# Kernel tuning notes

Measured on AMD Instinct MI355X. Metric: run time of the kernel, lower is better.

Reference implementation:

```python
import jax, jax.numpy as jnp
import numpy as np

B, NF, FD, ND, C, K, L = 32, 64, 64, 256, 8, 6, 2  # batch, num_frames(feat), fused_dim, nodes, edge channels, neighbors, layers


def setup_inputs() -> dict:
    key = jax.random.key(0)
    ks = jax.random.split(key, 6)
    s = lambda k, shape: jax.random.normal(k, shape, jnp.float32) * 0.05
    return {
        "fused": jax.random.normal(ks[0], (B, NF, FD), jnp.float32),
        "w1": s(ks[1], (NF, FD, FD)),
        "b1": jnp.zeros((NF, 1, FD), jnp.float32),
        "w2": s(ks[2], (NF, FD, ND)),
        "b2": jnp.zeros((NF, 1, ND), jnp.float32),
        "edge_qk_w": s(ks[3], (2 * C * NF, NF)),
        "ga_qk_w": s(ks[4], (L, 2 * NF, NF)),
        "ga_qk_b": jnp.zeros((L, 2 * NF), jnp.float32),
        "ga_w": jnp.ones((L, 1, C), jnp.float32),
    }


def _spec_norm(w):
    # per-node spectral normalization (torch does this in-place under no_grad)
    n = jax.lax.stop_gradient(jnp.linalg.norm(w, ord=2, axis=(1, 2), keepdims=True))
    return w / jnp.clip(n, 1e-6, None)


def _forward(fused, w1, b1, w2, b2, edge_qk_w, ga_qk_w, ga_qk_b, ga_w):
    scale = NF ** -0.5
    # --- MultiNodeMlp (per-frame node-wise MLP) ---
    h = jnp.einsum('bni,nij->bnj', fused, _spec_norm(w1)) + b1[:, 0]
    h = jax.nn.gelu(h, approximate=False)
    conv = jnp.einsum('bni,nio->bno', h, _spec_norm(w2)) + b2[:, 0]  # [B,NF,ND]
    x = conv.transpose(0, 2, 1)  # node features [B,ND,NF]

    # --- EdgeLayer: multi-channel attention + top-k clip + double normalization ---
    qk = (x @ edge_qk_w.T).reshape(B, ND, 2, C, NF)
    q = qk[:, :, 0].transpose(0, 2, 1, 3)  # [B,C,ND,NF]
    k = qk[:, :, 1].transpose(0, 2, 1, 3)
    attn = jax.nn.softmax(jnp.einsum('bcnf,bcmf->bcnm', q, k) * scale, axis=-1)
    sum_edge = jax.lax.stop_gradient(attn).sum(axis=1)            # [B,ND,ND]
    top_idx = jax.lax.top_k(sum_edge, K)[1]                       # [B,ND,K]
    onehot = jnp.clip(jax.nn.one_hot(top_idx, ND, dtype=attn.dtype).sum(axis=2), 0.0, 1.0)
    mask = jnp.maximum(onehot, jnp.eye(ND, dtype=attn.dtype))[:, None]  # [B,1,ND,ND]
    masked = mask * attn
    nr = masked / (masked.sum(-1, keepdims=True) + 1e-6)
    nc = nr / (nr.sum(-2, keepdims=True) + 1e-6)
    edge = jnp.einsum('bcnd,bcmd->bcnm', nr, nc)                  # norm_row @ norm_col^T

    # --- LipschitzGraph: residual invertible graph attention layers ---
    eye = jnp.eye(NF, dtype=x.dtype)
    for l in range(L):
        W, bqk, wch = ga_qk_w[l], ga_qk_b[l], ga_w[l]
        xs = jax.nn.sigmoid(jax.nn.elu(x))
        qkx = xs @ W.T + bqk                                       # [B,ND,2NF]
        qg, kg = qkx[..., :NF], qkx[..., NF:]
        a = jax.nn.softmax(jnp.einsum('bnf,bmf->bnm', qg, kg) * scale, axis=-1)
        ne = a[:, None] * edge                                     # [B,C,ND,ND]
        ne = ne / (ne.sum(-1, keepdims=True) + 1e-6)
        ne = jnp.einsum('bcnd,c->bnd', ne, (wch / wch.sum())[0])
        dot = W[:NF] @ W[NF:].T * scale
        lip = jax.lax.stop_gradient(jnp.linalg.norm(eye + 2.0 * dot, ord=2)) + 5.0
        x = x + (ne @ xs) / lip
    return x


def reference(fused, w1, b1, w2, b2, edge_qk_w, ga_qk_w, ga_qk_b, ga_w):
    return _forward(fused, w1, b1, w2, b2, edge_qk_w, ga_qk_w, ga_qk_b, ga_w)
```

## Files before the change

kernel.cpp:

```cpp
#include <hip/hip_runtime.h>
#include <float.h>
#include <math.h>


typedef short bf8t __attribute__((ext_vector_type(8)));
typedef float f4t __attribute__((ext_vector_type(4)));

static __device__ __forceinline__ unsigned short f2bf(float x) {
  union { float f; unsigned u; } v; v.f = x;
  unsigned r = (v.u + 0x7FFFu + ((v.u >> 16) & 1u)) >> 16;
  return (unsigned short)r;
}
static __device__ __forceinline__ float bf2f(unsigned short s) {
  union { unsigned u; float f; } v; v.u = ((unsigned)s) << 16; return v.f;
}
static __device__ __forceinline__ float bf2f_lo(unsigned u) {
  union { unsigned u; float f; } v; v.u = u << 16; return v.f;
}
static __device__ __forceinline__ float bf2f_hi(unsigned u) {
  union { unsigned u; float f; } v; v.u = u & 0xFFFF0000u; return v.f;
}
static __device__ __forceinline__ float dot3_pair(unsigned uqh, unsigned uql,
                                                  unsigned ukh, unsigned ukl) {
  float s = bf2f_lo(uqh) * (bf2f_lo(ukh) + bf2f_lo(ukl)) + bf2f_lo(uql) * bf2f_lo(ukh);
  s += bf2f_hi(uqh) * (bf2f_hi(ukh) + bf2f_hi(ukl)) + bf2f_hi(uql) * bf2f_hi(ukh);
  return s;
}
static __device__ __forceinline__ void split8(const float* __restrict__ p,
                                              bf8t* hi, bf8t* lo) {
  float4 v0 = *(const float4*)(p);
  float4 v1 = *(const float4*)(p + 4);
  float v[8] = {v0.x, v0.y, v0.z, v0.w, v1.x, v1.y, v1.z, v1.w};
#pragma unroll
  for (int j = 0; j < 8; j++) {
    unsigned short h = f2bf(v[j]);
    (*hi)[j] = (short)h;
    (*lo)[j] = (short)f2bf(v[j] - bf2f(h));
  }
}

#define SPAD 68

static __device__ __forceinline__ void mm_mfma(
    const float* __restrict__ A, const float* __restrict__ B,
    float* __restrict__ C, int t, float scale, int addI, int transposeStore) {
  int wv = t >> 6, l = t & 63;
  int m16 = l & 15, quad = l >> 4;
  bf8t ah[2], al[2];
  const float* ap = A + (size_t)(16 * wv + m16) * SPAD + quad * 8;
  split8(ap, &ah[0], &al[0]);
  split8(ap + 32, &ah[1], &al[1]);
  f4t acc[4];
#pragma unroll
  for (int ct = 0; ct < 4; ct++) {
    bf8t bh[2], bl[2];
    const float* bp = B + (size_t)(ct * 16 + m16) * SPAD + quad * 8;
    split8(bp, &bh[0], &bl[0]);
    split8(bp + 32, &bh[1], &bl[1]);
    f4t a = (f4t){0.f, 0.f, 0.f, 0.f};
    a = __builtin_amdgcn_mfma_f32_16x16x32_bf16(al[0], bh[0], a, 0, 0, 0);
    a = __builtin_amdgcn_mfma_f32_16x16x32_bf16(ah[0], bl[0], a, 0, 0, 0);
    a = __builtin_amdgcn_mfma_f32_16x16x32_bf16(ah[0], bh[0], a, 0, 0, 0);
    a = __builtin_amdgcn_mfma_f32_16x16x32_bf16(al[1], bh[1], a, 0, 0, 0);
    a = __builtin_amdgcn_mfma_f32_16x16x32_bf16(ah[1], bl[1], a, 0, 0, 0);
    a = __builtin_amdgcn_mfma_f32_16x16x32_bf16(ah[1], bh[1], a, 0, 0, 0);
    acc[ct] = a;
  }
#pragma unroll
  for (int ct = 0; ct < 4; ct++)
#pragma unroll
    for (int j = 0; j < 4; j++) {
      int i0 = 16 * wv + quad * 4 + j;
      int j0 = ct * 16 + m16;
      float v = acc[ct][j] * scale + ((addI && i0 == j0) ? 1.0f : 0.0f);
      if (transposeStore) C[(size_t)j0 * SPAD + i0] = v;
      else C[(size_t)i0 * SPAD + j0] = v;
    }
}

static __device__ __forceinline__ void mm_sq_norm(
    const float* __restrict__ A, float* __restrict__ C, int t,
    float* __restrict__ redm) {
  int wv = t >> 6, l = t & 63;
  int m16 = l & 15, quad = l >> 4;
  bf8t ah[2], al[2];
  const float* ap = A + (size_t)(16 * wv + m16) * SPAD + quad * 8;
  split8(ap, &ah[0], &al[0]);
  split8(ap + 32, &ah[1], &al[1]);
  f4t acc[4];
#pragma unroll
  for (int ct = 0; ct < 4; ct++) {
    bf8t bh[2], bl[2];
    const float* bp = A + (size_t)(ct * 16 + m16) * SPAD + quad * 8;
    split8(bp, &bh[0], &bl[0]);
    split8(bp + 32, &bh[1], &bl[1]);
    f4t a = (f4t){0.f, 0.f, 0.f, 0.f};
    a = __builtin_amdgcn_mfma_f32_16x16x32_bf16(al[0], bh[0], a, 0, 0, 0);
    a = __builtin_amdgcn_mfma_f32_16x16x32_bf16(ah[0], bl[0], a, 0, 0, 0);
    a = __builtin_amdgcn_mfma_f32_16x16x32_bf16(ah[0], bh[0], a, 0, 0, 0);
    a = __builtin_amdgcn_mfma_f32_16x16x32_bf16(al[1], bh[1], a, 0, 0, 0);
    a = __builtin_amdgcn_mfma_f32_16x16x32_bf16(ah[1], bl[1], a, 0, 0, 0);
    a = __builtin_amdgcn_mfma_f32_16x16x32_bf16(ah[1], bh[1], a, 0, 0, 0);
    acc[ct] = a;
  }
  float mx = 0.f;
#pragma unroll
  for (int ct = 0; ct < 4; ct++)
#pragma unroll
    for (int j = 0; j < 4; j++) mx = fmaxf(mx, fabsf(acc[ct][j]));
#pragma unroll
  for (int m = 1; m < 64; m <<= 1) mx = fmaxf(mx, __shfl_xor(mx, m, 64));
  if (l == 0) redm[wv] = mx;
  __syncthreads();
  float gmx = fmaxf(fmaxf(redm[0], redm[1]), fmaxf(redm[2], redm[3]));
  float sc = 1.0f / fmaxf(gmx, 1e-30f);
#pragma unroll
  for (int ct = 0; ct < 4; ct++)
#pragma unroll
    for (int j = 0; j < 4; j++)
      C[(size_t)(16 * wv + quad * 4 + j) * SPAD + ct * 16 + m16] = acc[ct][j] * sc;
}

static __device__ __forceinline__ void gram_mfma(
    const float* __restrict__ Ag, int ncols, float* __restrict__ S,
    float* __restrict__ G, int t) {
  int wv = t >> 6, l = t & 63;
  int m16 = l & 15, quad = l >> 4;
  f4t acc[4];
#pragma unroll
  for (int ct = 0; ct < 4; ct++) acc[ct] = (f4t){0.f, 0.f, 0.f, 0.f};
  for (int cc = 0; cc < ncols; cc += 64) {
    if (cc) __syncthreads();
    for (int i = t; i < 1024; i += 256) {
      int r = i >> 4, qq = i & 15;
      float4 v = *(const float4*)(Ag + (size_t)r * ncols + cc + 4 * qq);
      *(float4*)(S + (size_t)r * SPAD + 4 * qq) = v;
    }
    __syncthreads();
    bf8t ah[2], al[2];
    const float* ap = S + (size_t)(16 * wv + m16) * SPAD + quad * 8;
    split8(ap, &ah[0], &al[0]);
    split8(ap + 32, &ah[1], &al[1]);
#pragma unroll
    for (int ct = 0; ct < 4; ct++) {
      bf8t bh[2], bl[2];
      const float* bp = S + (size_t)(ct * 16 + m16) * SPAD + quad * 8;
      split8(bp, &bh[0], &bl[0]);
      split8(bp + 32, &bh[1], &bl[1]);
      f4t a = acc[ct];
      a = __builtin_amdgcn_mfma_f32_16x16x32_bf16(al[0], bh[0], a, 0, 0, 0);
      a = __builtin_amdgcn_mfma_f32_16x16x32_bf16(ah[0], bl[0], a, 0, 0, 0);
      a = __builtin_amdgcn_mfma_f32_16x16x32_bf16(ah[0], bh[0], a, 0, 0, 0);
      a = __builtin_amdgcn_mfma_f32_16x16x32_bf16(al[1], bh[1], a, 0, 0, 0);
      a = __builtin_amdgcn_mfma_f32_16x16x32_bf16(ah[1], bl[1], a, 0, 0, 0);
      a = __builtin_amdgcn_mfma_f32_16x16x32_bf16(ah[1], bh[1], a, 0, 0, 0);
      acc[ct] = a;
    }
  }
  __syncthreads();
#pragma unroll
  for (int ct = 0; ct < 4; ct++)
#pragma unroll
    for (int j = 0; j < 4; j++)
      G[(size_t)(16 * wv + quad * 4 + j) * SPAD + ct * 16 + m16] = acc[ct][j];
}

static __device__ __forceinline__ float power_rayleigh(
    const float* __restrict__ G4m, const float* __restrict__ Gm, int iters, int i) {
  float row[64];
#pragma unroll
  for (int j = 0; j < 16; j++)
    *(float4*)(row + 4 * j) = *(const float4*)(G4m + (size_t)i * SPAD + 4 * j);
  float v = 1.0f + 0.3f * sinf(7.0f * (float)(i + 1));
  for (int it = 0; it < iters; it++) {
    float u0 = 0.f, u1 = 0.f, u2 = 0.f, u3 = 0.f;
#pragma unroll
    for (int j = 0; j < 16; j++) {
      u0 += row[4 * j + 0] * __shfl(v, 4 * j + 0, 64);
      u1 += row[4 * j + 1] * __shfl(v, 4 * j + 1, 64);
      u2 += row[4 * j + 2] * __shfl(v, 4 * j + 2, 64);
      u3 += row[4 * j + 3] * __shfl(v, 4 * j + 3, 64);
    }
    float u = (u0 + u1) + (u2 + u3);
    float ss = u * u;
#pragma unroll
    for (int m = 1; m < 64; m <<= 1) ss += __shfl_xor(ss, m, 64);
    v = u * rsqrtf(fmaxf(ss, 1e-30f));
  }
  float rowg[64];
#pragma unroll
  for (int j = 0; j < 16; j++)
    *(float4*)(rowg + 4 * j) = *(const float4*)(Gm + (size_t)i * SPAD + 4 * j);
  float u0 = 0.f, u1 = 0.f, u2 = 0.f, u3 = 0.f;
#pragma unroll
  for (int j = 0; j < 16; j++) {
    u0 += rowg[4 * j + 0] * __shfl(v, 4 * j + 0, 64);
    u1 += rowg[4 * j + 1] * __shfl(v, 4 * j + 1, 64);
    u2 += rowg[4 * j + 2] * __shfl(v, 4 * j + 2, 64);
    u3 += rowg[4 * j + 3] * __shfl(v, 4 * j + 3, 64);
  }
  float u = (u0 + u1) + (u2 + u3);
  float d = v * u;
#pragma unroll
  for (int m = 1; m < 64; m <<= 1) d += __shfl_xor(d, m, 64);
  return d;
}

__global__ __launch_bounds__(256) void speclip_kernel(
    const float* __restrict__ w1, const float* __restrict__ w2,
    const float* __restrict__ gaw, float* __restrict__ invsig1,
    float* __restrict__ invsig2, float* __restrict__ lipv) {
  __shared__ float Sa[64 * SPAD];
  __shared__ float Sb[64 * SPAD];
  __shared__ float G[64 * SPAD];
  __shared__ float redm[4];
  int t = threadIdx.x;
  int blk = blockIdx.x;
  if (blk < 128) {
    int n = blk & 63;
    const float* A = (blk < 64) ? (w1 + (size_t)n * 4096) : (w2 + (size_t)n * 16384);
    int ncols = (blk < 64) ? 64 : 256;
    gram_mfma(A, ncols, Sa, G, t);
    __syncthreads();
    mm_mfma(G, G, Sa, t, 1.f, 0, 0);
    __syncthreads();
    mm_sq_norm(Sa, Sb, t, redm);  __syncthreads();
    mm_sq_norm(Sb, Sa, t, redm);  __syncthreads();
    mm_sq_norm(Sa, Sb, t, redm);  __syncthreads();
    mm_sq_norm(Sb, Sa, t, redm);  __syncthreads();
    mm_sq_norm(Sa, Sb, t, redm);  __syncthreads();
    mm_sq_norm(Sb, Sa, t, redm);  __syncthreads();
    if (t < 64) {
      float d = power_rayleigh(Sa, G, 2, t);
      if (t == 0) {
        float sg = sqrtf(fmaxf(d, 0.f));
        float inv = 1.0f / fmaxf(sg, 1e-6f);
        if (blk < 64) invsig1[n] = inv; else invsig2[n] = inv;
      }
    }
  } else {
    int l = blk - 128;
    const float* Wb = gaw + (size_t)l * 8192;
    for (int i = t; i < 1024; i += 256) {
      int r = i >> 4, qq = i & 15;
      *(float4*)(Sa + (size_t)r * SPAD + 4 * qq) = *(const float4*)(Wb + r * 64 + 4 * qq);
      *(float4*)(Sb + (size_t)r * SPAD + 4 * qq) = *(const float4*)(Wb + 4096 + r * 64 + 4 * qq);
    }
    __syncthreads();
    mm_mfma(Sa, Sb, G, t, 0.25f, 1, 1);
    __syncthreads();
    mm_mfma(G, G, Sa, t, 1.f, 0, 0);
    __syncthreads();
    mm_sq_norm(Sa, Sb, t, redm);  __syncthreads();
    mm_sq_norm(Sb, G, t, redm);   __syncthreads();
    mm_sq_norm(G, Sb, t, redm);   __syncthreads();
    mm_sq_norm(Sb, G, t, redm);   __syncthreads();
    mm_sq_norm(G, Sb, t, redm);   __syncthreads();
    mm_sq_norm(Sb, G, t, redm);   __syncthreads();
    if (t < 64) {
      float d = power_rayleigh(G, Sa, 2, t);
      if (t == 0) lipv[l] = sqrtf(fmaxf(d, 0.f)) + 5.0f;
    }
  }
}

__global__ __launch_bounds__(256) void h_kernel(
    const float* __restrict__ fused, const float* __restrict__ w1,
    const float* __restrict__ b1, const float* __restrict__ invsig1,
    float* __restrict__ h) {
  __shared__ float fr[256];
  int t = threadIdx.x;
  int blk = blockIdx.x;
  int ng = blk & 15;
  fr[t] = fused[(size_t)blk * 256 + t];
  __syncthreads();
  int nl = t >> 6, j = t & 63;
  int n = ng * 4 + nl;
  float is1 = invsig1[n];
  const float* fp = fr + nl * 64;
  const float* wp = w1 + (size_t)n * 4096 + j;
  float acc = 0.f;
  for (int i = 0; i < 64; i++) acc += fp[i] * wp[i * 64];
  acc = acc * is1 + b1[n * 64 + j];
  float g = 0.5f * acc * (1.0f + erff(acc * 0.70710678118654752440f));
  h[(size_t)blk * 256 + t] = g;
}

__global__ __launch_bounds__(256) void conv_kernel(
    const float* __restrict__ h, const float* __restrict__ w2,
    const float* __restrict__ b2, const float* __restrict__ invsig2,
    float* __restrict__ x) {
  __shared__ float hr[4][64];
  int t = threadIdx.x;
  int blk = blockIdx.x;
  int b = blk >> 4, ng = blk & 15;
  int n0 = ng * 4;
  {
    int r = t >> 6, i = t & 63;
    hr[r][i] = h[((size_t)b * 64 + n0 + r) * 64 + i];
  }
  __syncthreads();
  const float* w0p = w2 + ((size_t)(n0 + 0) * 64) * 256 + t;
  const float* w1p = w2 + ((size_t)(n0 + 1) * 64) * 256 + t;
  const float* w2p = w2 + ((size_t)(n0 + 2) * 64) * 256 + t;
  const float* w3p = w2 + ((size_t)(n0 + 3) * 64) * 256 + t;
  float a0 = 0.f, a1 = 0.f, a2 = 0.f, a3 = 0.f;
  for (int i = 0; i < 64; i++) {
    a0 += hr[0][i] * w0p[(size_t)i * 256];
    a1 += hr[1][i] * w1p[(size_t)i * 256];
    a2 += hr[2][i] * w2p[(size_t)i * 256];
    a3 += hr[3][i] * w3p[(size_t)i * 256];
  }
  float4 o;
  o.x = a0 * invsig2[n0 + 0] + b2[(n0 + 0) * 256 + t];
  o.y = a1 * invsig2[n0 + 1] + b2[(n0 + 1) * 256 + t];
  o.z = a2 * invsig2[n0 + 2] + b2[(n0 + 2) * 256 + t];
  o.w = a3 * invsig2[n0 + 3] + b2[(n0 + 3) * 256 + t];
  *(float4*)(x + ((size_t)b * 256 + t) * 64 + n0) = o;
}

__global__ __launch_bounds__(256, 2) void qk_kernel(
    const float* __restrict__ x, const float* __restrict__ eqk,
    unsigned short* __restrict__ qhi, unsigned short* __restrict__ qlo,
    unsigned short* __restrict__ khi, unsigned short* __restrict__ klo) {
  int t = threadIdx.x;
  int blk = blockIdx.x;
  int xcd = blk & 7;
  int y = blk >> 3;
  int rh = y & 1;
  int c = (y >> 1) & 7;
  int b = (y >> 4) * 8 + xcd;
  int wv = t >> 6, l = t & 63;
  int m16 = l & 15, quad = l >> 4;
  int row0 = rh * 128 + wv * 32;

  bf8t ah[2][2], al[2][2];
#pragma unroll
  for (int rt = 0; rt < 2; rt++) {
    const float* xp = x + ((size_t)b * 256 + row0 + rt * 16 + m16) * 64 + quad * 8;
    split8(xp, &ah[rt][0], &al[rt][0]);
    split8(xp + 32, &ah[rt][1], &al[rt][1]);
  }
#pragma unroll
  for (int mat = 0; mat < 2; mat++) {
    const float* Wbase = eqk + ((size_t)(mat * 8 + c) * 64) * 64;
    unsigned short* ohi = mat ? khi : qhi;
    unsigned short* olo = mat ? klo : qlo;
#pragma unroll
    for (int ct = 0; ct < 4; ct++) {
      bf8t bh[2], bl[2];
      const float* wp = Wbase + (size_t)(ct * 16 + m16) * 64 + quad * 8;
      split8(wp, &bh[0], &bl[0]);
      split8(wp + 32, &bh[1], &bl[1]);
#pragma unroll
      for (int rt = 0; rt < 2; rt++) {
        f4t a = (f4t){0.f, 0.f, 0.f, 0.f};
        a = __builtin_amdgcn_mfma_f32_16x16x32_bf16(al[rt][0], bh[0], a, 0, 0, 0);
        a = __builtin_amdgcn_mfma_f32_16x16x32_bf16(ah[rt][0], bl[0], a, 0, 0, 0);
        a = __builtin_amdgcn_mfma_f32_16x16x32_bf16(ah[rt][0], bh[0], a, 0, 0, 0);
        a = __builtin_amdgcn_mfma_f32_16x16x32_bf16(al[rt][1], bh[1], a, 0, 0, 0);
        a = __builtin_amdgcn_mfma_f32_16x16x32_bf16(ah[rt][1], bl[1], a, 0, 0, 0);
        a = __builtin_amdgcn_mfma_f32_16x16x32_bf16(ah[rt][1], bh[1], a, 0, 0, 0);
#pragma unroll
        for (int j = 0; j < 4; j++) {
          int n = row0 + rt * 16 + quad * 4 + j;
          int f = ct * 16 + m16;
          size_t o = (((size_t)b * 8 + c) * 256 + n) * 64 + f;
          float v = a[j];
          unsigned short hh = f2bf(v);
          ohi[o] = hh;
          olo[o] = f2bf(v - bf2f(hh));
        }
      }
    }
  }
}

__global__ __launch_bounds__(256, 2) void transpose_kernel(
    const float* __restrict__ in, float* __restrict__ out) {
  __shared__ float T[256 * 65];
  int t = threadIdx.x;
  size_t base = (size_t)blockIdx.x * 16384;
  const float4* in4 = (const float4*)(in + base);
  float4* out4 = (float4*)(out + base);
  for (int i = t; i < 4096; i += 256) {
    int n = i >> 4, fq = i & 15;
    float4 v = in4[i];
    float* dst = T + n * 65 + 4 * fq;
    dst[0] = v.x; dst[1] = v.y; dst[2] = v.z; dst[3] = v.w;
  }
  __syncthreads();
  for (int i = t; i < 4096; i += 256) {
    int f = i >> 6, m4 = i & 63;
    float4 o;
    o.x = T[(4 * m4 + 0) * 65 + f];
    o.y = T[(4 * m4 + 1) * 65 + f];
    o.z = T[(4 * m4 + 2) * 65 + f];
    o.w = T[(4 * m4 + 3) * 65 + f];
    out4[f * 64 + m4] = o;
  }
}

__global__ __launch_bounds__(512, 4) void attn_kernel(
    const unsigned short* __restrict__ qhi, const unsigned short* __restrict__ qlo,
    const unsigned short* __restrict__ khi, const unsigned short* __restrict__ klo,
    float* __restrict__ seP, float* __restrict__ mxb, float* __restrict__ rzb) {
  __shared__ uint4 KS4[4096];
  unsigned short* KS = (unsigned short*)KS4;
  float* sE = (float*)KS4;
  int t = threadIdx.x;
  int blk = blockIdx.x;
  int xcd = blk & 7;
  int y = blk >> 3;
  int b = xcd * 4 + (y & 3);
  int cg = (y >> 2) & 3;
  int ng = y >> 4;
  int wave = t >> 6;
  int ci = wave >> 2;
  int wv = wave & 3;
  int l = t & 63;
  int m16 = l & 15, quad = l >> 4;
  int n0w = ng * 64 + wv * 16;
  int c = cg * 2 + ci;

  size_t slA = ((size_t)b * 8 + cg * 2) * 16384;
  size_t slB = slA + 16384;
  size_t sl = ((size_t)b * 8 + c) * 16384;

  const bf8t* qh = (const bf8t*)(qhi + sl + (size_t)(n0w + m16) * 64 + quad * 8);
  const bf8t* ql = (const bf8t*)(qlo + sl + (size_t)(n0w + m16) * 64 + quad * 8);
  bf8t ah0 = qh[0], ah1 = qh[4];
  bf8t al0 = ql[0], al1 = ql[4];

  int sthalf = (t >> 6) & 1;
  int tllo = (t >> 7) & 3;
  int srcbase = tllo * 1024 + m16 * 64 + sthalf * 32 + quad * 8;
  int dstbase = t * 8;

  int lane8 = (quad * 16 + m16) * 8;
  int cbase = ci * 16384;

  f4t acc[16];
#pragma unroll
  for (int mt = 0; mt < 16; mt++) acc[mt] = (f4t){0.f, 0.f, 0.f, 0.f};

#pragma unroll
  for (int p = 0; p < 2; p++) {
    if (p) __syncthreads();
    int pb = srcbase + p * 8192;
#pragma unroll
    for (int g = 0; g < 2; g++) {
      const unsigned short* bhp = khi + (g ? slB : slA) + pb;
      const unsigned short* blp = klo + (g ? slB : slA) + pb;
      uint4 v0 = *(const uint4*)(bhp);
      uint4 v1 = *(const uint4*)(bhp + 4096);
      uint4 v2 = *(const uint4*)(blp);
      uint4 v3 = *(const uint4*)(blp + 4096);
      *(uint4*)(KS + dstbase + (g * 4 + 0) * 4096) = v0;
      *(uint4*)(KS + dstbase + (g * 4 + 1) * 4096) = v1;
      *(uint4*)(KS + dstbase + (g * 4 + 2) * 4096) = v2;
      *(uint4*)(KS + dstbase + (g * 4 + 3) * 4096) = v3;
    }
    __syncthreads();
#pragma unroll
    for (int tl = 0; tl < 8; tl++) {
      int mt = p * 8 + tl;
      int tb = cbase + tl * 1024 + lane8;
      bf8t bh0 = *(const bf8t*)(KS + tb);
      bf8t bh1 = *(const bf8t*)(KS + tb + 512);
      bf8t bl0 = *(const bf8t*)(KS + tb + 8192);
      bf8t bl1 = *(const bf8t*)(KS + tb + 8704);
      f4t a = acc[mt];
      a = __builtin_amdgcn_mfma_f32_16x16x32_bf16(al0, bh0, a, 0, 0, 0);
      a = __builtin_amdgcn_mfma_f32_16x16x32_bf16(ah0, bl0, a, 0, 0, 0);
      a = __builtin_amdgcn_mfma_f32_16x16x32_bf16(ah0, bh0, a, 0, 0, 0);
      a = __builtin_amdgcn_mfma_f32_16x16x32_bf16(al1, bh1, a, 0, 0, 0);
      a = __builtin_amdgcn_mfma_f32_16x16x32_bf16(ah1, bl1, a, 0, 0, 0);
      a = __builtin_amdgcn_mfma_f32_16x16x32_bf16(ah1, bh1, a, 0, 0, 0);
      acc[mt] = a;
    }
  }
#pragma unroll
  for (int j = 0; j < 4; j++) {
    float mx = -FLT_MAX;
#pragma unroll
    for (int mt = 0; mt < 16; mt++) mx = fmaxf(mx, acc[mt][j]);
    mx = fmaxf(mx, __shfl_xor(mx, 1, 64));
    mx = fmaxf(mx, __shfl_xor(mx, 2, 64));
    mx = fmaxf(mx, __shfl_xor(mx, 4, 64));
    mx = fmaxf(mx, __shfl_xor(mx, 8, 64));
    float mxl = mx * 0.125f;
    float z = 0.f;
#pragma unroll
    for (int mt = 0; mt < 16; mt++) {
      float e = expf(acc[mt][j] * 0.125f - mxl);
      acc[mt][j] = e;
      z += e;
    }
    z += __shfl_xor(z, 1, 64);
    z += __shfl_xor(z, 2, 64);
    z += __shfl_xor(z, 4, 64);
    z += __shfl_xor(z, 8, 64);
    int n = n0w + quad * 4 + j;
    if (m16 == 0) {
      mxb[((size_t)b * 8 + c) * 256 + n] = mxl;
      rzb[((size_t)b * 8 + c) * 256 + n] = z;
    }
    float zi = 1.0f / z;
#pragma unroll
    for (int mt = 0; mt < 16; mt++) acc[mt][j] *= zi;
  }
  __syncthreads();
  for (int half = 0; half < 2; half++) {
    if (ci == 0 && (wv >> 1) == half) {
      int r0 = (wv & 1) * 16;
#pragma unroll
      for (int mt = 0; mt < 16; mt++)
#pragma unroll
        for (int j = 0; j < 4; j++)
          sE[(r0 + quad * 4 + j) * 260 + mt * 16 + m16] = acc[mt][j];
    }
    __syncthreads();
    if (ci == 1 && (wv >> 1) == half) {
      int r0 = (wv & 1) * 16;
#pragma unroll
      for (int mt = 0; mt < 16; mt++)
#pragma unroll
        for (int j = 0; j < 4; j++)
          sE[(r0 + quad * 4 + j) * 260 + mt * 16 + m16] += acc[mt][j];
    }
    __syncthreads();
    float4* dst4 = (float4*)(seP + (((size_t)cg * 32 + b) * 256 + ng * 64 + half * 32) * 256);
    for (int i = t; i < 2048; i += 512) {
      int r = i >> 6, c4 = i & 63;
      dst4[i] = *(const float4*)(sE + r * 260 + c4 * 4);
    }
    if (half == 0) __syncthreads();
  }
}

__global__ __launch_bounds__(256) void topsel_kernel(
    const float* __restrict__ seP, int* __restrict__ idx7) {
  __shared__ float seL[64 * 260];
  __shared__ float cv[64][24];
  __shared__ int cidx[64][24];
  int t = threadIdx.x;
  int b = blockIdx.x >> 2, rg = blockIdx.x & 3;
  int n0 = rg * 64;
  const float* s0 = seP + ((size_t)b * 256 + n0) * 256;
  const float* s1 = seP + ((size_t)(32 + b) * 256 + n0) * 256;
  const float* s2 = seP + ((size_t)(64 + b) * 256 + n0) * 256;
  const float* s3 = seP + ((size_t)(96 + b) * 256 + n0) * 256;
  for (int i = t; i < 4096; i += 256) {
    int m4 = i & 63, r = i >> 6;
    float4 v0 = ((const float4*)(s0 + (size_t)r * 256))[m4];
    float4 v1 = ((const float4*)(s1 + (size_t)r * 256))[m4];
    float4 v2 = ((const float4*)(s2 + (size_t)r * 256))[m4];
    float4 v3 = ((const float4*)(s3 + (size_t)r * 256))[m4];
    float4 s;
    s.x = (v0.x + v1.x) + (v2.x + v3.x);
    s.y = (v0.y + v1.y) + (v2.y + v3.y);
    s.z = (v0.z + v1.z) + (v2.z + v3.z);
    s.w = (v0.w + v1.w) + (v2.w + v3.w);
    *(float4*)(seL + r * 260 + m4 * 4) = s;
  }
  __syncthreads();
  {
    int r = t >> 2, qtr = t & 3;
    float tv[6]; int ti[6];
#pragma unroll
    for (int s = 0; s < 6; s++) { tv[s] = -FLT_MAX; ti[s] = 1 << 30; }
    for (int i = 0; i < 64; i++) {
      int m = 4 * i + qtr;
      float val = seL[r * 260 + m];
      if (val > tv[5]) {
        tv[5] = val; ti[5] = m;
#pragma unroll
        for (int s = 5; s > 0; s--) {
          if (tv[s] > tv[s - 1]) {
            float tmv = tv[s]; tv[s] = tv[s - 1]; tv[s - 1] = tmv;
            int tmi = ti[s]; ti[s] = ti[s - 1]; ti[s - 1] = tmi;
          }
        }
      }
    }
#pragma unroll
    for (int s = 0; s < 6; s++) { cv[r][qtr * 6 + s] = tv[s]; cidx[r][qtr * 6 + s] = ti[s]; }
  }
  __syncthreads();
  if (t < 64) {
    int r = t, n = n0 + r;
    int sel[7];
    for (int round = 0; round < 6; round++) {
      float best = -FLT_MAX; int bi = 1 << 30, bs = 0;
      for (int j = 0; j < 24; j++) {
        float v = cv[r][j]; int id = cidx[r][j];
        if (v > best || (v == best && id < bi)) { best = v; bi = id; bs = j; }
      }
      sel[round] = bi;
      cv[r][bs] = -FLT_MAX;
    }
    bool dup = false;
#pragma unroll
    for (int j = 0; j < 6; j++) dup = dup || (sel[j] == n);
    sel[6] = dup ? -1 : n;
#pragma unroll
    for (int j = 0; j < 7; j++) idx7[((size_t)b * 256 + n) * 7 + j] = sel[j];
  }
}

__global__ __launch_bounds__(256) void nr_kernel(
    const unsigned short* __restrict__ qhi, const unsigned short* __restrict__ qlo,
    const unsigned short* __restrict__ khi, const unsigned short* __restrict__ klo,
    const float* __restrict__ mxb, const float* __restrict__ rzb,
    const int* __restrict__ idx7, float* __restrict__ nrv,
    float* __restrict__ colsum) {
  __shared__ int idxs[7];
  __shared__ float attL[56];
  int t = threadIdx.x;
  int b = blockIdx.x >> 8, n = blockIdx.x & 255;
  if (t < 7) idxs[t] = idx7[(size_t)blockIdx.x * 7 + t];
  __syncthreads();
  int task = t >> 2, l4 = t & 3;
  if (task < 56) {
    int c = task / 7, j = task - c * 7;
    int d = idxs[j];
    float s = 0.f;
    if (d >= 0) {
      size_t qo = (((size_t)b * 8 + c) * 256 + n) * 64 + l4 * 16;
      size_t ko = (((size_t)b * 8 + c) * 256 + d) * 64 + l4 * 16;
      const uint4* qh4 = (const uint4*)(qhi + qo);
      const uint4* ql4 = (const uint4*)(qlo + qo);
      const uint4* kh4 = (const uint4*)(khi + ko);
      const uint4* kl4 = (const uint4*)(klo + ko);
#pragma unroll
      for (int g = 0; g < 2; g++) {
        uint4 uqh = qh4[g], uql = ql4[g], ukh = kh4[g], ukl = kl4[g];
        s += dot3_pair(uqh.x, uql.x, ukh.x, ukl.x);
        s += dot3_pair(uqh.y, uql.y, ukh.y, ukl.y);
        s += dot3_pair(uqh.z, uql.z, ukh.z, ukl.z);
        s += dot3_pair(uqh.w, uql.w, ukh.w, ukl.w);
      }
    }
    s += __shfl_xor(s, 1, 64);
    s += __shfl_xor(s, 2, 64);
    if (l4 == 0) {
      float att = 0.f;
      if (d >= 0) {
        float logit = s * 0.125f;
        att = expf(logit - mxb[((size_t)b * 8 + c) * 256 + n]) / rzb[((size_t)b * 8 + c) * 256 + n];
      }
      attL[task] = att;
    }
  }
  __syncthreads();
  if (t < 8) {
    float rs = 0.f;
#pragma unroll
    for (int j = 0; j < 7; j++) rs += attL[t * 7 + j];
    float ri = 1.0f / (rs + 1e-6f);
#pragma unroll
    for (int j = 0; j < 7; j++) {
      float nv = attL[t * 7 + j] * ri;
      nrv[(((size_t)b * 8 + t) * 256 + n) * 7 + j] = nv;
      int d = idxs[j];
      if (d >= 0) atomicAdd(&colsum[((size_t)b * 8 + t) * 256 + d], nv);
    }
  }
}

__global__ __launch_bounds__(256, 3) void edge_kernel(
    const int* __restrict__ idx7, const float* __restrict__ nrv,
    const float* __restrict__ colsum, unsigned short* __restrict__ edge) {
  __shared__ unsigned short ncT[256 * 64];
  __shared__ short idxL[256 * 8];
  __shared__ float nrvL[256 * 8];
  int t = threadIdx.x;
  int blk = blockIdx.x;
  int b = blk >> 5, c = (blk >> 2) & 7, mq = blk & 3;
  int m0 = mq * 64;
  for (int i = t; i < 8192; i += 256) ((unsigned int*)ncT)[i] = 0u;
  for (int i = t; i < 2048; i += 256) {
    int r = i >> 3, j = i & 7;
    if (j < 7) {
      idxL[i] = (short)idx7[(size_t)b * 1792 + r * 7 + j];
      nrvL[i] = nrv[((size_t)b * 8 + c) * 1792 + r * 7 + j];
    } else {
      idxL[i] = -1;
      nrvL[i] = 0.f;
    }
  }
  __syncthreads();
  for (int i = t; i < 448; i += 256) {
    int mi = i / 7, j = i - mi * 7;
    int m = m0 + mi;
    int d = idxL[m * 8 + j];
    if (d >= 0) {
      float cs = colsum[((size_t)b * 8 + c) * 256 + d];
      ncT[d * 64 + mi] = f2bf(nrvL[m * 8 + j] / (cs + 1e-6f));
    }
  }
  __syncthreads();
  int wv = t >> 6, l = t & 63;
  int half = l >> 5, p = l & 31;
  const unsigned int* ncP = (const unsigned int*)ncT;
  unsigned int* eb = (unsigned int*)(edge + (((size_t)b * 8 + c) * 256) * 256);
  for (int nn = 0; nn < 32; nn++) {
    int n = nn * 8 + wv * 2 + half;
    int4 iv = *(const int4*)(idxL + n * 8);
    float4 w0 = *(const float4*)(nrvL + n * 8);
    float4 w1 = *(const float4*)(nrvL + n * 8 + 4);
    float a0 = 0.f, a1 = 0.f;
    int d;
    unsigned int pr;
    d = (int)(short)(iv.x & 0xFFFF);
    if (d >= 0) { pr = ncP[d * 32 + p]; a0 += w0.x * bf2f_lo(pr); a1 += w0.x * bf2f_hi(pr); }
    d = iv.x >> 16;
    if (d >= 0) { pr = ncP[d * 32 + p]; a0 += w0.y * bf2f_lo(pr); a1 += w0.y * bf2f_hi(pr); }
    d = (int)(short)(iv.y & 0xFFFF);
    if (d >= 0) { pr = ncP[d * 32 + p]; a0 += w0.z * bf2f_lo(pr); a1 += w0.z * bf2f_hi(pr); }
    d = iv.y >> 16;
    if (d >= 0) { pr = ncP[d * 32 + p]; a0 += w0.w * bf2f_lo(pr); a1 += w0.w * bf2f_hi(pr); }
    d = (int)(short)(iv.z & 0xFFFF);
    if (d >= 0) { pr = ncP[d * 32 + p]; a0 += w1.x * bf2f_lo(pr); a1 += w1.x * bf2f_hi(pr); }
    d = iv.z >> 16;
    if (d >= 0) { pr = ncP[d * 32 + p]; a0 += w1.y * bf2f_lo(pr); a1 += w1.y * bf2f_hi(pr); }
    d = (int)(short)(iv.w & 0xFFFF);
    if (d >= 0) { pr = ncP[d * 32 + p]; a0 += w1.z * bf2f_lo(pr); a1 += w1.z * bf2f_hi(pr); }
    unsigned int packo = (unsigned int)f2bf(a0) | ((unsigned int)f2bf(a1) << 16);
    eb[n * 128 + (m0 >> 1) + p] = packo;
  }
}

static __device__ __forceinline__ float selu1(float v) {
  float e = (v > 0.f) ? v : expm1f(v);
  return 1.0f / (1.0f + expf(-e));
}
__global__ __launch_bounds__(256, 1) void qkx_kernel(
    const float* __restrict__ x, const float* __restrict__ gaw,
    const float* __restrict__ gab, int l, float* __restrict__ xs,
    float* __restrict__ qg, float* __restrict__ kg) {
  __shared__ float xsL[64 * 64];
  int t = threadIdx.x;
  int b = blockIdx.x >> 2, nt = blockIdx.x & 3;
  int f = t & 63, part = t >> 6;
  float wq[64], wk[64];
  const float4* Wq4 = (const float4*)(gaw + (size_t)l * 8192 + f * 64);
  const float4* Wk4 = (const float4*)(gaw + (size_t)l * 8192 + (64 + f) * 64);
#pragma unroll
  for (int j = 0; j < 16; j++) {
    float4 aa = Wq4[j];
    wq[4 * j + 0] = aa.x; wq[4 * j + 1] = aa.y; wq[4 * j + 2] = aa.z; wq[4 * j + 3] = aa.w;
    float4 bb = Wk4[j];
    wk[4 * j + 0] = bb.x; wk[4 * j + 1] = bb.y; wk[4 * j + 2] = bb.z; wk[4 * j + 3] = bb.w;
  }
  float bq = gab[l * 128 + f], bk = gab[l * 128 + 64 + f];
  for (int i = t; i < 1024; i += 256) {
    float4 v = ((const float4*)(x + ((size_t)b * 256 + nt * 64) * 64))[i];
    float4 o;
    o.x = selu1(v.x); o.y = selu1(v.y); o.z = selu1(v.z); o.w = selu1(v.w);
    ((float4*)xsL)[i] = o;
    ((float4*)(xs + ((size_t)b * 256 + nt * 64) * 64))[i] = o;
  }
  __syncthreads();
  for (int i = 0; i < 16; i++) {
    int nl = part * 16 + i;
    const float4* xr = (const float4*)(xsL + nl * 64);
    float aq = 0.f, ak = 0.f;
#pragma unroll
    for (int j = 0; j < 16; j++) {
      float4 v = xr[j];
      aq += v.x * wq[4 * j] + v.y * wq[4 * j + 1] + v.z * wq[4 * j + 2] + v.w * wq[4 * j + 3];
      ak += v.x * wk[4 * j] + v.y * wk[4 * j + 1] + v.z * wk[4 * j + 2] + v.w * wk[4 * j + 3];
    }
    int n = nt * 64 + nl;
    qg[((size_t)b * 256 + n) * 64 + f] = aq + bq;
    kg[((size_t)b * 256 + n) * 64 + f] = ak + bk;
  }
}

__global__ __launch_bounds__(256, 2) void ga_attn_kernel(
    const float* __restrict__ qg, const float* __restrict__ kgT,
    float* __restrict__ a) {
  int t = threadIdx.x;
  int b = blockIdx.x >> 3, nt = blockIdx.x & 7;
  int n0 = nt * 32;
  int wv = t >> 6, l = t & 63;
  const float* kb = kgT + (size_t)b * 16384 + 4 * l;
  const float* qb = qg + ((size_t)b * 256 + n0 + wv * 8) * 64;
  float acc[8][4];
#pragma unroll
  for (int r = 0; r < 8; r++)
#pragma unroll
    for (int j = 0; j < 4; j++) acc[r][j] = 0.f;
#pragma unroll 4
  for (int kq4 = 0; kq4 < 64; kq4 += 4) {
    float4 kv0 = *(const float4*)(kb + (kq4 + 0) * 256);
    float4 kv1 = *(const float4*)(kb + (kq4 + 1) * 256);
    float4 kv2 = *(const float4*)(kb + (kq4 + 2) * 256);
    float4 kv3 = *(const float4*)(kb + (kq4 + 3) * 256);
#pragma unroll
    for (int r = 0; r < 8; r++) {
      float4 qv = *(const float4*)(qb + r * 64 + kq4);
      acc[r][0] += qv.x * kv0.x + qv.y * kv1.x + qv.z * kv2.x + qv.w * kv3.x;
      acc[r][1] += qv.x * kv0.y + qv.y * kv1.y + qv.z * kv2.y + qv.w * kv3.y;
      acc[r][2] += qv.x * kv0.z + qv.y * kv1.z + qv.z * kv2.z + qv.w * kv3.z;
      acc[r][3] += qv.x * kv0.w + qv.y * kv1.w + qv.z * kv2.w + qv.w * kv3.w;
    }
  }
#pragma unroll
  for (int r = 0; r < 8; r++) {
    float l0 = acc[r][0] * 0.125f, l1 = acc[r][1] * 0.125f;
    float l2 = acc[r][2] * 0.125f, l3 = acc[r][3] * 0.125f;
    float mx = fmaxf(fmaxf(l0, l1), fmaxf(l2, l3));
#pragma unroll
    for (int m = 1; m < 64; m <<= 1) mx = fmaxf(mx, __shfl_xor(mx, m, 64));
    float e0 = expf(l0 - mx), e1 = expf(l1 - mx), e2 = expf(l2 - mx), e3 = expf(l3 - mx);
    float z = e0 + e1 + e2 + e3;
#pragma unroll
    for (int m = 1; m < 64; m <<= 1) z += __shfl_xor(z, m, 64);
    float zi = 1.0f / z;
    int n = n0 + wv * 8 + r;
    float4 o;
    o.x = e0 * zi; o.y = e1 * zi; o.z = e2 * zi; o.w = e3 * zi;
    ((float4*)(a + ((size_t)b * 256 + n) * 256))[l] = o;
  }
}

__global__ __launch_bounds__(256) void upd_kernel(
    const float* __restrict__ a, const unsigned short* __restrict__ edge,
    const float* __restrict__ xs, const float* __restrict__ gaww,
    const float* __restrict__ lipv, int l, float* __restrict__ x) {
  __shared__ float tt[4][8][260];
  __shared__ float ne3[4][256];
  __shared__ float parts[4][4][64];
  __shared__ float dred[32][8];
  __shared__ float dinv[4][8];
  __shared__ float wcL[8];
  __shared__ float lipi;
  int t = threadIdx.x;
  int b = blockIdx.x >> 6, nq = blockIdx.x & 63;
  int n0 = nq * 4;
  if (t == 0) {
    float s = 0.f;
    float wtmp[8];
    for (int c = 0; c < 8; c++) { wtmp[c] = gaww[l * 8 + c]; s += wtmp[c]; }
    for (int c = 0; c < 8; c++) wcL[c] = wtmp[c] / s;
    lipi = 1.0f / lipv[l];
  }
#pragma unroll
  for (int r = 0; r < 4; r++) {
    float av = a[((size_t)b * 256 + n0 + r) * 256 + t];
#pragma unroll
    for (int c = 0; c < 8; c++)
      tt[r][c][t] = av * bf2f(edge[(((size_t)b * 8 + c) * 256 + n0 + r) * 256 + t]);
  }
  __syncthreads();
  {
    int rc = t >> 3, i = t & 7;
    int r = rc >> 3, c = rc & 7;
    float p = 0.f;
#pragma unroll
    for (int kq = 0; kq < 32; kq++) p += tt[r][c][i + 8 * kq];
    dred[rc][i] = p;
  }
  __syncthreads();
  if (t < 32) {
    float s = 0.f;
#pragma unroll
    for (int i = 0; i < 8; i++) s += dred[t][i];
    dinv[t >> 3][t & 7] = 1.0f / (s + 1e-6f);
  }
  __syncthreads();
#pragma unroll
  for (int r = 0; r < 4; r++) {
    float s = 0.f;
#pragma unroll
    for (int c = 0; c < 8; c++) s += wcL[c] * tt[r][c][t] * dinv[r][c];
    ne3[r][t] = s;
  }
  __syncthreads();
  {
    int f = t & 63, part = t >> 6;
    float a0 = 0.f, a1 = 0.f, a2 = 0.f, a3 = 0.f;
    for (int mm = 0; mm < 64; mm++) {
      int m = part * 64 + mm;
      float xv = xs[((size_t)b * 256 + m) * 64 + f];
      a0 += ne3[0][m] * xv;
      a1 += ne3[1][m] * xv;
      a2 += ne3[2][m] * xv;
      a3 += ne3[3][m] * xv;
    }
    parts[0][part][f] = a0;
    parts[1][part][f] = a1;
    parts[2][part][f] = a2;
    parts[3][part][f] = a3;
  }
  __syncthreads();
  {
    int r = t >> 6, f = t & 63;
    float dx = parts[r][0][f] + parts[r][1][f] + parts[r][2][f] + parts[r][3][f];
    x[((size_t)b * 256 + n0 + r) * 64 + f] += dx * lipi;
  }
}

extern "C" void kernel_launch(void* const* d_in, const int* in_sizes, int n_in,
                              void* d_out, int out_size, void* d_ws, size_t ws_size,
                              hipStream_t stream) {
  (void)in_sizes; (void)n_in; (void)out_size; (void)ws_size;
  const float* fused = (const float*)d_in[0];
  const float* w1 = (const float*)d_in[1];
  const float* b1 = (const float*)d_in[2];
  const float* w2 = (const float*)d_in[3];
  const float* b2 = (const float*)d_in[4];
  const float* eqk = (const float*)d_in[5];
  const float* gaw = (const float*)d_in[6];
  const float* gab = (const float*)d_in[7];
  const float* gaww = (const float*)d_in[8];
  float* x = (float*)d_out;
  char* ws = (char*)d_ws;
  size_t off = 0;
  auto alloc = [&](size_t bytes) -> char* {
    char* p = ws + off;
    off += (bytes + 1023) & ~(size_t)1023;
    return p;
  };
  float* invsig1 = (float*)alloc(64 * 4);
  float* invsig2 = (float*)alloc(64 * 4);
  float* lipv = (float*)alloc(2 * 4);
  float* h = (float*)alloc((size_t)32 * 64 * 64 * 4);
  unsigned short* qhi = (unsigned short*)alloc((size_t)32 * 8 * 256 * 64 * 2);
  unsigned short* qlo = (unsigned short*)alloc((size_t)32 * 8 * 256 * 64 * 2);
  unsigned short* khi = (unsigned short*)alloc((size_t)32 * 8 * 256 * 64 * 2);
  unsigned short* klo = (unsigned short*)alloc((size_t)32 * 8 * 256 * 64 * 2);
  char* sep_edge = alloc((size_t)4 * 32 * 256 * 256 * 4);
  float* seP = (float*)sep_edge;
  unsigned short* edge = (unsigned short*)sep_edge;
  float* mxb = (float*)alloc((size_t)65536 * 4);
  float* rzb = (float*)alloc((size_t)65536 * 4);
  int* idx7 = (int*)alloc((size_t)8192 * 7 * 4);
  float* nrv = (float*)alloc((size_t)65536 * 7 * 4);
  float* colsum = (float*)alloc((size_t)65536 * 4);
  float* xs = (float*)alloc((size_t)524288 * 4);
  float* qg = (float*)alloc((size_t)524288 * 4);
  float* kg = (float*)alloc((size_t)524288 * 4);
  float* a = (float*)alloc((size_t)32 * 256 * 256 * 4);
  float* kgT = (float*)alloc((size_t)524288 * 4);

  speclip_kernel<<<130, 256, 0, stream>>>(w1, w2, gaw, invsig1, invsig2, lipv);
  h_kernel<<<512, 256, 0, stream>>>(fused, w1, b1, invsig1, h);
  conv_kernel<<<512, 256, 0, stream>>>(h, w2, b2, invsig2, x);
  qk_kernel<<<512, 256, 0, stream>>>(x, eqk, qhi, qlo, khi, klo);
  attn_kernel<<<512, 512, 0, stream>>>(qhi, qlo, khi, klo, seP, mxb, rzb);
  hipMemsetAsync(colsum, 0, (size_t)65536 * 4, stream);
  topsel_kernel<<<128, 256, 0, stream>>>(seP, idx7);
  nr_kernel<<<8192, 256, 0, stream>>>(qhi, qlo, khi, klo, mxb, rzb, idx7, nrv, colsum);
  edge_kernel<<<1024, 256, 0, stream>>>(idx7, nrv, colsum, edge);
  for (int l = 0; l < 2; l++) {
    qkx_kernel<<<128, 256, 0, stream>>>(x, gaw, gab, l, xs, qg, kg);
    transpose_kernel<<<32, 256, 0, stream>>>(kg, kgT);
    ga_attn_kernel<<<256, 256, 0, stream>>>(qg, kgT, a);
    upd_kernel<<<2048, 256, 0, stream>>>(a, edge, xs, gaww, lipv, l, x);
  }
}
```

Before: 373.6 us.

## Fuse MLP stages, fold k transpose into qkx, prefetch second K tile in attn

Merges h_kernel and conv_kernel into a single kernel that keeps the GELU hidden activations in shared memory rather than writing them to a global buffer. The qkx kernel now writes k already transposed through a padded shared tile, which removes the separate transpose launch in each graph layer. In attn_kernel, the global loads for the second K half are issued before the MFMAs on the first half, so load latency overlaps compute. The cost is higher register pressure from holding 16 uint4 staging registers, which may lower occupancy at 512 threads.

```diff
diff --git a/kernel.cpp b/kernel.cpp
--- a/kernel.cpp
+++ b/kernel.cpp
@@ -264,40 +264,29 @@
   }
 }
 
-__global__ __launch_bounds__(256) void h_kernel(
+__global__ __launch_bounds__(256) void hconv_kernel(
     const float* __restrict__ fused, const float* __restrict__ w1,
     const float* __restrict__ b1, const float* __restrict__ invsig1,
-    float* __restrict__ h) {
+    const float* __restrict__ w2, const float* __restrict__ b2,
+    const float* __restrict__ invsig2, float* __restrict__ x) {
   __shared__ float fr[256];
-  int t = threadIdx.x;
-  int blk = blockIdx.x;
-  int ng = blk & 15;
-  fr[t] = fused[(size_t)blk * 256 + t];
-  __syncthreads();
-  int nl = t >> 6, j = t & 63;
-  int n = ng * 4 + nl;
-  float is1 = invsig1[n];
-  const float* fp = fr + nl * 64;
-  const float* wp = w1 + (size_t)n * 4096 + j;
-  float acc = 0.f;
-  for (int i = 0; i < 64; i++) acc += fp[i] * wp[i * 64];
-  acc = acc * is1 + b1[n * 64 + j];
-  float g = 0.5f * acc * (1.0f + erff(acc * 0.70710678118654752440f));
-  h[(size_t)blk * 256 + t] = g;
-}
-
-__global__ __launch_bounds__(256) void conv_kernel(
-    const float* __restrict__ h, const float* __restrict__ w2,
-    const float* __restrict__ b2, const float* __restrict__ invsig2,
-    float* __restrict__ x) {
   __shared__ float hr[4][64];
   int t = threadIdx.x;
   int blk = blockIdx.x;
   int b = blk >> 4, ng = blk & 15;
   int n0 = ng * 4;
+  fr[t] = fused[(size_t)blk * 256 + t];
+  __syncthreads();
   {
-    int r = t >> 6, i = t & 63;
-    hr[r][i] = h[((size_t)b * 64 + n0 + r) * 64 + i];
+    int nl = t >> 6, j = t & 63;
+    int n = n0 + nl;
+    float is1 = invsig1[n];
+    const float* fp = fr + nl * 64;
+    const float* wp = w1 + (size_t)n * 4096 + j;
+    float acc = 0.f;
+    for (int i = 0; i < 64; i++) acc += fp[i] * wp[i * 64];
+    acc = acc * is1 + b1[n * 64 + j];
+    hr[nl][j] = 0.5f * acc * (1.0f + erff(acc * 0.70710678118654752440f));
   }
   __syncthreads();
   const float* w0p = w2 + ((size_t)(n0 + 0) * 64) * 256 + t;
@@ -373,31 +362,6 @@
         }
       }
     }
-  }
-}
-
-__global__ __launch_bounds__(256, 2) void transpose_kernel(
-    const float* __restrict__ in, float* __restrict__ out) {
-  __shared__ float T[256 * 65];
-  int t = threadIdx.x;
-  size_t base = (size_t)blockIdx.x * 16384;
-  const float4* in4 = (const float4*)(in + base);
-  float4* out4 = (float4*)(out + base);
-  for (int i = t; i < 4096; i += 256) {
-    int n = i >> 4, fq = i & 15;
-    float4 v = in4[i];
-    float* dst = T + n * 65 + 4 * fq;
-    dst[0] = v.x; dst[1] = v.y; dst[2] = v.z; dst[3] = v.w;
-  }
-  __syncthreads();
-  for (int i = t; i < 4096; i += 256) {
-    int f = i >> 6, m4 = i & 63;
-    float4 o;
-    o.x = T[(4 * m4 + 0) * 65 + f];
-    o.y = T[(4 * m4 + 1) * 65 + f];
-    o.z = T[(4 * m4 + 2) * 65 + f];
-    o.w = T[(4 * m4 + 3) * 65 + f];
-    out4[f * 64 + m4] = o;
   }
 }
 
@@ -444,41 +408,69 @@
 #pragma unroll
   for (int mt = 0; mt < 16; mt++) acc[mt] = (f4t){0.f, 0.f, 0.f, 0.f};
 
-#pragma unroll
-  for (int p = 0; p < 2; p++) {
-    if (p) __syncthreads();
-    int pb = srcbase + p * 8192;
+  uint4 va[8], vb[8];
+  {
+    int pb = srcbase;
 #pragma unroll
     for (int g = 0; g < 2; g++) {
       const unsigned short* bhp = khi + (g ? slB : slA) + pb;
       const unsigned short* blp = klo + (g ? slB : slA) + pb;
-      uint4 v0 = *(const uint4*)(bhp);
-      uint4 v1 = *(const uint4*)(bhp + 4096);
-      uint4 v2 = *(const uint4*)(blp);
-      uint4 v3 = *(const uint4*)(blp + 4096);
-      *(uint4*)(KS + dstbase + (g * 4 + 0) * 4096) = v0;
-      *(uint4*)(KS + dstbase + (g * 4 + 1) * 4096) = v1;
-      *(uint4*)(KS + dstbase + (g * 4 + 2) * 4096) = v2;
-      *(uint4*)(KS + dstbase + (g * 4 + 3) * 4096) = v3;
-    }
-    __syncthreads();
-#pragma unroll
-    for (int tl = 0; tl < 8; tl++) {
-      int mt = p * 8 + tl;
-      int tb = cbase + tl * 1024 + lane8;
-      bf8t bh0 = *(const bf8t*)(KS + tb);
-      bf8t bh1 = *(const bf8t*)(KS + tb + 512);
-      bf8t bl0 = *(const bf8t*)(KS + tb + 8192);
-      bf8t bl1 = *(const bf8t*)(KS + tb + 8704);
-      f4t a = acc[mt];
-      a = __builtin_amdgcn_mfma_f32_16x16x32_bf16(al0, bh0, a, 0, 0, 0);
-      a = __builtin_amdgcn_mfma_f32_16x16x32_bf16(ah0, bl0, a, 0, 0, 0);
-      a = __builtin_amdgcn_mfma_f32_16x16x32_bf16(ah0, bh0, a, 0, 0, 0);
-      a = __builtin_amdgcn_mfma_f32_16x16x32_bf16(al1, bh1, a, 0, 0, 0);
-      a = __builtin_amdgcn_mfma_f32_16x16x32_bf16(ah1, bl1, a, 0, 0, 0);
-      a = __builtin_amdgcn_mfma_f32_16x16x32_bf16(ah1, bh1, a, 0, 0, 0);
-      acc[mt] = a;
-    }
+      va[g * 4 + 0] = *(const uint4*)(bhp);
+      va[g * 4 + 1] = *(const uint4*)(bhp + 4096);
+      va[g * 4 + 2] = *(const uint4*)(blp);
+      va[g * 4 + 3] = *(const uint4*)(blp + 4096);
+    }
+  }
+#pragma unroll
+  for (int it = 0; it < 8; it++) *(uint4*)(KS + dstbase + it * 4096) = va[it];
+  __syncthreads();
+  {
+    int pb = srcbase + 8192;
+#pragma unroll
+    for (int g = 0; g < 2; g++) {
+      const unsigned short* bhp = khi + (g ? slB : slA) + pb;
+      const unsigned short* blp = klo + (g ? slB : slA) + pb;
+      vb[g * 4 + 0] = *(const uint4*)(bhp);
+      vb[g * 4 + 1] = *(const uint4*)(bhp + 4096);
+      vb[g * 4 + 2] = *(const uint4*)(blp);
+      vb[g * 4 + 3] = *(const uint4*)(blp + 4096);
+    }
+  }
+#pragma unroll
+  for (int tl = 0; tl < 8; tl++) {
+    int tb = cbase + tl * 1024 + lane8;
+    bf8t bh0 = *(const bf8t*)(KS + tb);
+    bf8t bh1 = *(const bf8t*)(KS + tb + 512);
+    bf8t bl0 = *(const bf8t*)(KS + tb + 8192);
+    bf8t bl1 = *(const bf8t*)(KS + tb + 8704);
+    f4t a = acc[tl];
+    a = __builtin_amdgcn_mfma_f32_16x16x32_bf16(al0, bh0, a, 0, 0, 0);
+    a = __builtin_amdgcn_mfma_f32_16x16x32_bf16(ah0, bl0, a, 0, 0, 0);
+    a = __builtin_amdgcn_mfma_f32_16x16x32_bf16(ah0, bh0, a, 0, 0, 0);
+    a = __builtin_amdgcn_mfma_f32_16x16x32_bf16(al1, bh1, a, 0, 0, 0);
+    a = __builtin_amdgcn_mfma_f32_16x16x32_bf16(ah1, bl1, a, 0, 0, 0);
+    a = __builtin_amdgcn_mfma_f32_16x16x32_bf16(ah1, bh1, a, 0, 0, 0);
+    acc[tl] = a;
+  }
+  __syncthreads();
+#pragma unroll
+  for (int it = 0; it < 8; it++) *(uint4*)(KS + dstbase + it * 4096) = vb[it];
+  __syncthreads();
+#pragma unroll
+  for (int tl = 0; tl < 8; tl++) {
+    int tb = cbase + tl * 1024 + lane8;
+    bf8t bh0 = *(const bf8t*)(KS + tb);
+    bf8t bh1 = *(const bf8t*)(KS + tb + 512);
+    bf8t bl0 = *(const bf8t*)(KS + tb + 8192);
+    bf8t bl1 = *(const bf8t*)(KS + tb + 8704);
+    f4t a = acc[8 + tl];
+    a = __builtin_amdgcn_mfma_f32_16x16x32_bf16(al0, bh0, a, 0, 0, 0);
+    a = __builtin_amdgcn_mfma_f32_16x16x32_bf16(ah0, bl0, a, 0, 0, 0);
+    a = __builtin_amdgcn_mfma_f32_16x16x32_bf16(ah0, bh0, a, 0, 0, 0);
+    a = __builtin_amdgcn_mfma_f32_16x16x32_bf16(al1, bh1, a, 0, 0, 0);
+    a = __builtin_amdgcn_mfma_f32_16x16x32_bf16(ah1, bl1, a, 0, 0, 0);
+    a = __builtin_amdgcn_mfma_f32_16x16x32_bf16(ah1, bh1, a, 0, 0, 0);
+    acc[8 + tl] = a;
   }
 #pragma unroll
   for (int j = 0; j < 4; j++) {
@@ -739,8 +731,9 @@
 __global__ __launch_bounds__(256, 1) void qkx_kernel(
     const float* __restrict__ x, const float* __restrict__ gaw,
     const float* __restrict__ gab, int l, float* __restrict__ xs,
-    float* __restrict__ qg, float* __restrict__ kg) {
+    float* __restrict__ qg, float* __restrict__ kgT) {
   __shared__ float xsL[64 * 64];
+  __shared__ float kT[64][65];
   int t = threadIdx.x;
   int b = blockIdx.x >> 2, nt = blockIdx.x & 3;
   int f = t & 63, part = t >> 6;
@@ -775,7 +768,17 @@
     }
     int n = nt * 64 + nl;
     qg[((size_t)b * 256 + n) * 64 + f] = aq + bq;
-    kg[((size_t)b * 256 + n) * 64 + f] = ak + bk;
+    kT[f][nl] = ak + bk;
+  }
+  __syncthreads();
+  for (int i = t; i < 1024; i += 256) {
+    int ff = i >> 4, qq = i & 15;
+    float4 o;
+    o.x = kT[ff][4 * qq + 0];
+    o.y = kT[ff][4 * qq + 1];
+    o.z = kT[ff][4 * qq + 2];
+    o.w = kT[ff][4 * qq + 3];
+    *(float4*)(kgT + (size_t)b * 16384 + ff * 256 + nt * 64 + 4 * qq) = o;
   }
 }
 
@@ -928,7 +931,6 @@
   float* invsig1 = (float*)alloc(64 * 4);
   float* invsig2 = (float*)alloc(64 * 4);
   float* lipv = (float*)alloc(2 * 4);
-  float* h = (float*)alloc((size_t)32 * 64 * 64 * 4);
   unsigned short* qhi = (unsigned short*)alloc((size_t)32 * 8 * 256 * 64 * 2);
   unsigned short* qlo = (unsigned short*)alloc((size_t)32 * 8 * 256 * 64 * 2);
   unsigned short* khi = (unsigned short*)alloc((size_t)32 * 8 * 256 * 64 * 2);
@@ -943,13 +945,11 @@
   float* colsum = (float*)alloc((size_t)65536 * 4);
   float* xs = (float*)alloc((size_t)524288 * 4);
   float* qg = (float*)alloc((size_t)524288 * 4);
-  float* kg = (float*)alloc((size_t)524288 * 4);
   float* a = (float*)alloc((size_t)32 * 256 * 256 * 4);
   float* kgT = (float*)alloc((size_t)524288 * 4);
 
   speclip_kernel<<<130, 256, 0, stream>>>(w1, w2, gaw, invsig1, invsig2, lipv);
-  h_kernel<<<512, 256, 0, stream>>>(fused, w1, b1, invsig1, h);
-  conv_kernel<<<512, 256, 0, stream>>>(h, w2, b2, invsig2, x);
+  hconv_kernel<<<512, 256, 0, stream>>>(fused, w1, b1, invsig1, w2, b2, invsig2, x);
   qk_kernel<<<512, 256, 0, stream>>>(x, eqk, qhi, qlo, khi, klo);
   attn_kernel<<<512, 512, 0, stream>>>(qhi, qlo, khi, klo, seP, mxb, rzb);
   hipMemsetAsync(colsum, 0, (size_t)65536 * 4, stream);
@@ -957,8 +957,7 @@
   nr_kernel<<<8192, 256, 0, stream>>>(qhi, qlo, khi, klo, mxb, rzb, idx7, nrv, colsum);
   edge_kernel<<<1024, 256, 0, stream>>>(idx7, nrv, colsum, edge);
   for (int l = 0; l < 2; l++) {
-    qkx_kernel<<<128, 256, 0, stream>>>(x, gaw, gab, l, xs, qg, kg);
-    transpose_kernel<<<32, 256, 0, stream>>>(kg, kgT);
+    qkx_kernel<<<128, 256, 0, stream>>>(x, gaw, gab, l, xs, qg, kgT);
     ga_attn_kernel<<<256, 256, 0, stream>>>(qg, kgT, a);
     upd_kernel<<<2048, 256, 0, stream>>>(a, edge, xs, gaww, lipv, l, x);
   }
```

Result: slower. 382.4 us (+2.4%).
